# Performance work log

Hardware: AMD Instinct MI355X
Metric: run time of the kernel (lower is better)

Reference implementation:

```python
import jax, jax.numpy as jnp
import numpy as np

N = 1_000_000
B = 4096
L = 4
CC = 3
K = (L + 1) ** 2  # 25


def setup_inputs() -> dict:
    key = jax.random.key(0)
    ks = jax.random.split(key, 20)
    points = jax.random.normal(ks[0], (N, 3), dtype=jnp.float32)
    color = jax.random.uniform(ks[1], (N, 3), dtype=jnp.float32)
    batch = jnp.sort(jax.random.randint(ks[2], (N,), 0, B, dtype=jnp.int64))

    def lin(k, o, i, s):
        return jax.random.normal(k, (o, i), dtype=jnp.float32) * s

    inp = {
        "points": points,
        "color": color,
        "batch": batch,
        # FeatureNet 1x1 conv weights (kernel size 1 -> plain linear)
        "w1": lin(ks[3], 32, 6, 0.4), "b1": jnp.zeros((32,), jnp.float32),
        "w2": lin(ks[4], 128, 32, 0.18), "b2": jnp.zeros((128,), jnp.float32),
        "w3": lin(ks[5], 256, 128, 0.09), "b3": jnp.zeros((256,), jnp.float32),
        # FC head
        "fw1": lin(ks[6], 128, 256, 0.06), "fb1": jnp.zeros((128,), jnp.float32),
        "fw2": lin(ks[7], 64, 128, 0.09), "fb2": jnp.zeros((64,), jnp.float32),
        "fw3": lin(ks[8], K * CC, 64, 0.12), "fb3": jnp.zeros((K * CC,), jnp.float32),
        "coef_mean": jnp.zeros((K, CC), jnp.float32),
        "coef_std": jnp.ones((K, CC), jnp.float32),
    }
    return inp


def reference(points, color, batch, w1, b1, w2, b2, w3, b3,
              fw1, fb1, fw2, fb2, fw3, fb3, coef_mean, coef_std):
    # per-point shared MLP (1x1 convs == linear over channel dim)
    x = jnp.concatenate([points, color], axis=-1)          # [N, 6]
    x = jax.nn.relu(x @ w1.T + b1)                          # [N, 32]
    x = jax.nn.relu(x @ w2.T + b2)                          # [N, 128]
    x = x @ w3.T + b3                                       # [N, 256]
    # scatter_reduce(amax) onto a zeros-initialized target (include_self=True)
    # => per-segment max clamped below at 0; empty segments stay 0.
    seg = jax.ops.segment_max(x, batch, num_segments=B, indices_are_sorted=True)
    x_max = jnp.maximum(seg, 0.0)                           # [B, 256]
    # FC head
    h = jax.nn.relu(x_max @ fw1.T + fb1)                    # [B, 128]
    h = jax.nn.relu(h @ fw2.T + fb2)                        # [B, 64]
    h = h @ fw3.T + fb3                                     # [B, 75]
    out = h.reshape(-1, K, CC) * coef_std + coef_mean       # [B, 25, 3]
    return out
```

## Files before the change

### kernel.cpp

```cpp
#include <hip/hip_runtime.h>
#include <hip/hip_bf16.h>

typedef __attribute__((ext_vector_type(8))) short short8;
typedef __attribute__((ext_vector_type(16))) float f32x16;

union U8 { short8 s; unsigned int u[4]; };

static __device__ __forceinline__ unsigned short f2bf(float f) {
  unsigned int u = __float_as_uint(f);
  u += 0x7fffu + ((u >> 16) & 1u);
  return (unsigned short)(u >> 16);
}
static __device__ __forceinline__ unsigned int cvtpk(float lo, float hi) {
  unsigned int r;
  asm("v_cvt_pk_bf16_f32 %0, %1, %2" : "=v"(r) : "v"(lo), "v"(hi));
  return r;
}
static __device__ __forceinline__ f32x16 MFMA(short8 a, short8 b, f32x16 c) {
  return __builtin_amdgcn_mfma_f32_32x32x16_bf16(a, b, c, 0, 0, 0);
}

__global__ void prep_weights(const float* __restrict__ w1, const float* __restrict__ w2,
                             const float* __restrict__ w3,
                             unsigned short* __restrict__ w1p, unsigned short* __restrict__ w2b,
                             unsigned short* __restrict__ w3b) {
  int i = blockIdx.x * 256 + threadIdx.x;
  if (i < 512) { int c = i >> 4, k = i & 15; w1p[i] = (k < 6) ? f2bf(w1[c * 6 + k]) : (unsigned short)0; }
  if (i < 4096) w2b[i] = f2bf(w2[i]);
  if (i < 32768) w3b[i] = f2bf(w3[i]);
}

__global__ __launch_bounds__(256, 2) void mlp_segmax_mfma(
    const float* __restrict__ points, const float* __restrict__ color,
    const int* __restrict__ batch,
    const unsigned short* __restrict__ w1p, const unsigned short* __restrict__ w2b,
    const unsigned short* __restrict__ w3b,
    const float* __restrict__ b1, const float* __restrict__ b2, const float* __restrict__ b3,
    float* __restrict__ xmax, int N)
{
  __shared__ __align__(16) char smem[73728];
  const int tid  = threadIdx.x;
  const int wv   = tid >> 6;
  const int lane = tid & 63;
  const int g    = lane >> 5;
  const int l31  = lane & 31;
  char* h2base = smem + wv * 16384;
  char* h1base = smem + 65536 + wv * 2048;

  float b1v[16];
#pragma unroll
  for (int r = 0; r < 16; ++r) b1v[r] = b1[(r & 3) + 8 * (r >> 2) + 4 * g];
  unsigned int b2pk[32];
#pragma unroll
  for (int t2 = 0; t2 < 4; ++t2)
#pragma unroll
    for (int q = 0; q < 4; ++q)
#pragma unroll
      for (int h = 0; h < 2; ++h) {
        int ch = 32 * t2 + 8 * q + 4 * g + 2 * h;
        b2pk[t2 * 8 + q * 2 + h] = (unsigned)f2bf(b2[ch]) | ((unsigned)f2bf(b2[ch + 1]) << 16);
      }
  float b3v[8];
#pragma unroll
  for (int t = 0; t < 8; ++t) b3v[t] = b3[32 * t + l31];

  const int wid = blockIdx.x * 4 + wv;
  const long long pstart = (long long)wid * 512;
  int cur = -1;
  float rmax[8];
#pragma unroll
  for (int t = 0; t < 8; ++t) rmax[t] = -INFINITY;

  auto flush = [&]() {
#pragma unroll
    for (int t = 0; t < 8; ++t) {
      float v = fmaxf(rmax[t], __shfl_xor(rmax[t], 32));
      if (lane < 32)
        atomicMax((int*)xmax + cur * 256 + 32 * t + lane, __float_as_int(v));
    }
  };

  for (int it = 0; it < 8; ++it) {
    const long long p0 = pstart + (long long)it * 64;
    if (p0 >= N) break;

    unsigned long long a1p = (unsigned long long)w1p; asm volatile("" : "+s"(a1p));
    unsigned long long a2p = (unsigned long long)w2b; asm volatile("" : "+s"(a2p));
    unsigned long long a3p = (unsigned long long)w3b; asm volatile("" : "+s"(a3p));
    const unsigned short* w1l = (const unsigned short*)a1p;
    const unsigned short* w2l = (const unsigned short*)a2p;
    const unsigned short* w3l = (const unsigned short*)a3p;

#pragma unroll
    for (int s2 = 0; s2 < 2; ++s2) {
      const int p = (int)p0 + 32 * s2 + l31;
      float px = points[p * 3 + 0], py = points[p * 3 + 1], pz = points[p * 3 + 2];
      float cr = color[p * 3 + 0],  cg = color[p * 3 + 1],  cbv = color[p * 3 + 2];
      unsigned int zm = (g == 0) ? 0xffffffffu : 0u;
      U8 bin;
      bin.u[0] = cvtpk(px, py) & zm;
      bin.u[1] = cvtpk(pz, cr) & zm;
      bin.u[2] = cvtpk(cg, cbv) & zm;
      bin.u[3] = 0;
      short8 a1 = *reinterpret_cast<const short8*>(w1l + l31 * 16 + 8 * g);
      f32x16 c1;
#pragma unroll
      for (int r = 0; r < 16; ++r) c1[r] = b1v[r];
      f32x16 d1 = MFMA(a1, bin.s, c1);
#pragma unroll
      for (int q = 0; q < 4; ++q) {
        float f0 = fmaxf(d1[q * 4 + 0], 0.f), f1 = fmaxf(d1[q * 4 + 1], 0.f);
        float f2 = fmaxf(d1[q * 4 + 2], 0.f), f3 = fmaxf(d1[q * 4 + 3], 0.f);
        uint2 w; w.x = cvtpk(f0, f1); w.y = cvtpk(f2, f3);
        *reinterpret_cast<uint2*>(h1base + l31 * 64 + ((q ^ (l31 & 3)) << 4) + 8 * g) = w;
      }
      short8 h1f0 = *reinterpret_cast<const short8*>(h1base + l31 * 64 + (((0 + g) ^ (l31 & 3)) << 4));
      short8 h1f1 = *reinterpret_cast<const short8*>(h1base + l31 * 64 + (((2 + g) ^ (l31 & 3)) << 4));
      const int row = 32 * s2 + l31;
#pragma unroll
      for (int t2 = 0; t2 < 4; ++t2) {
        f32x16 c2;
#pragma unroll
        for (int q = 0; q < 4; ++q) {
          unsigned int pka = b2pk[t2 * 8 + q * 2 + 0], pkb = b2pk[t2 * 8 + q * 2 + 1];
          c2[q * 4 + 0] = __uint_as_float(pka << 16);
          c2[q * 4 + 1] = __uint_as_float(pka & 0xffff0000u);
          c2[q * 4 + 2] = __uint_as_float(pkb << 16);
          c2[q * 4 + 3] = __uint_as_float(pkb & 0xffff0000u);
        }
        short8 a20 = *reinterpret_cast<const short8*>(w2l + (l31 + 32 * t2) * 32 + 8 * g);
        short8 a21 = *reinterpret_cast<const short8*>(w2l + (l31 + 32 * t2) * 32 + 16 + 8 * g);
        f32x16 d2 = MFMA(a20, h1f0, c2);
        d2 = MFMA(a21, h1f1, d2);
#pragma unroll
        for (int q = 0; q < 4; ++q) {
          float f0 = fmaxf(d2[q * 4 + 0], 0.f), f1 = fmaxf(d2[q * 4 + 1], 0.f);
          float f2 = fmaxf(d2[q * 4 + 2], 0.f), f3 = fmaxf(d2[q * 4 + 3], 0.f);
          uint2 w; w.x = cvtpk(f0, f1); w.y = cvtpk(f2, f3);
          int slot = q + 4 * t2;
          *reinterpret_cast<uint2*>(h2base + row * 256 + ((slot ^ (row & 15)) << 4) + 8 * g) = w;
        }
      }
    }

    short8 a3[2][8];
#pragma unroll
    for (int s2 = 0; s2 < 2; ++s2) {
      const int row = 32 * s2 + l31;
#pragma unroll
      for (int k0 = 0; k0 < 8; ++k0)
        a3[s2][k0] = *reinterpret_cast<const short8*>(
            h2base + row * 256 + (((2 * k0 + g) ^ (row & 15)) << 4));
    }

    const int segA = __builtin_amdgcn_readfirstlane(batch[p0]);
    const int segD = __builtin_amdgcn_readfirstlane(batch[p0 + 63]);
    const bool caseU = (segA == segD);
    unsigned int bitsA0 = 0, bitsD0 = 0, bitsA1 = 0, bitsD1 = 0;
    if (caseU) {
      if (segA != cur) {
        if (cur >= 0) flush();
        cur = segA;
#pragma unroll
        for (int t = 0; t < 8; ++t) rmax[t] = -INFINITY;
      }
    } else {
      if (cur >= 0 && cur != segA) flush();
      if (cur != segA) {
#pragma unroll
        for (int t = 0; t < 8; ++t) rmax[t] = -INFINITY;
        cur = segA;
      }
#pragma unroll
      for (int s2 = 0; s2 < 2; ++s2) {
        unsigned int bA = 0, bD = 0;
#pragma unroll
        for (int r = 0; r < 16; ++r) {
          int pr = (int)p0 + 32 * s2 + (r & 3) + 8 * (r >> 2) + 4 * g;
          int bs = batch[pr];
          bA |= (bs == segA) ? (1u << r) : 0u;
          bD |= (bs == segD) ? (1u << r) : 0u;
        }
        if (s2 == 0) { bitsA0 = bA; bitsD0 = bD; } else { bitsA1 = bA; bitsD1 = bD; }
      }
    }

    float m_a[8], m_d[8];
#pragma unroll
    for (int t = 0; t < 8; ++t) {
      f32x16 acc0, acc1;
#pragma unroll
      for (int r = 0; r < 16; ++r) { acc0[r] = b3v[t]; acc1[r] = b3v[t]; }
#pragma unroll
      for (int hh = 0; hh < 2; ++hh) {
        short8 bf[4];
#pragma unroll
        for (int k = 0; k < 4; ++k)
          bf[k] = *reinterpret_cast<const short8*>(
              w3l + (l31 + 32 * t) * 128 + (4 * hh + k) * 16 + 8 * g);
#pragma unroll
        for (int k = 0; k < 4; ++k) {
          acc0 = MFMA(a3[0][4 * hh + k], bf[k], acc0);
          acc1 = MFMA(a3[1][4 * hh + k], bf[k], acc1);
        }
      }
      if (caseU) {
        float m = acc0[0];
#pragma unroll
        for (int r = 1; r < 16; ++r) m = fmaxf(m, acc0[r]);
#pragma unroll
        for (int r = 0; r < 16; ++r) m = fmaxf(m, acc1[r]);
        rmax[t] = fmaxf(rmax[t], m);
      } else {
        float ma = -INFINITY, md = -INFINITY;
#pragma unroll
        for (int r = 0; r < 16; ++r) {
          float v0 = acc0[r], v1 = acc1[r];
          ma = fmaxf(ma, ((bitsA0 >> r) & 1) ? v0 : -INFINITY);
          md = fmaxf(md, ((bitsD0 >> r) & 1) ? v0 : -INFINITY);
          ma = fmaxf(ma, ((bitsA1 >> r) & 1) ? v1 : -INFINITY);
          md = fmaxf(md, ((bitsD1 >> r) & 1) ? v1 : -INFINITY);
        }
        unsigned int rest0 = (~(bitsA0 | bitsD0)) & 0xffffu;
        if (rest0) {
#pragma unroll
          for (int r = 0; r < 16; ++r) if ((rest0 >> r) & 1) {
            int pr = (int)p0 + (r & 3) + 8 * (r >> 2) + 4 * g;
            atomicMax((int*)xmax + batch[pr] * 256 + 32 * t + l31, __float_as_int(acc0[r]));
          }
        }
        unsigned int rest1 = (~(bitsA1 | bitsD1)) & 0xffffu;
        if (rest1) {
#pragma unroll
          for (int r = 0; r < 16; ++r) if ((rest1 >> r) & 1) {
            int pr = (int)p0 + 32 + (r & 3) + 8 * (r >> 2) + 4 * g;
            atomicMax((int*)xmax + batch[pr] * 256 + 32 * t + l31, __float_as_int(acc1[r]));
          }
        }
        m_a[t] = ma; m_d[t] = md;
      }
    }
    if (!caseU) {
#pragma unroll
      for (int t = 0; t < 8; ++t) rmax[t] = fmaxf(rmax[t], m_a[t]);
      flush();
      cur = segD;
#pragma unroll
      for (int t = 0; t < 8; ++t) rmax[t] = m_d[t];
    }
  }
  if (cur >= 0) flush();
}

__global__ __launch_bounds__(256) void head_kernel(
    const float* __restrict__ xmax,
    const float* __restrict__ fw1, const float* __restrict__ fb1,
    const float* __restrict__ fw2, const float* __restrict__ fb2,
    const float* __restrict__ fw3, const float* __restrict__ fb3,
    const float* __restrict__ cmean, const float* __restrict__ cstd,
    float* __restrict__ out, int B)
{
  __shared__ __align__(16) float xm[16][260];
  __shared__ __align__(16) float h1b[16][132];
  __shared__ __align__(16) float h2b[16][68];

  const int t = threadIdx.x;
  const int bbase = blockIdx.x * 16;

  for (int i = t; i < 16 * 256; i += 256) {
    const int bi = i >> 8, k = i & 255;
    const int bb = min(bbase + bi, B - 1);
    xm[bi][k] = xmax[(long long)bb * 256 + k];
  }
  __syncthreads();

  {
    const int bi = t >> 4, oi = t & 15;
    float acc[8];
#pragma unroll
    for (int u = 0; u < 8; ++u) acc[u] = fb1[oi * 8 + u];
    for (int k = 0; k < 256; k += 4) {
      const float4 xv = *reinterpret_cast<const float4*>(&xm[bi][k]);
#pragma unroll
      for (int u = 0; u < 8; ++u) {
        const float4 wv = *reinterpret_cast<const float4*>(fw1 + (oi * 8 + u) * 256 + k);
        acc[u] = fmaf(xv.x, wv.x, acc[u]);
        acc[u] = fmaf(xv.y, wv.y, acc[u]);
        acc[u] = fmaf(xv.z, wv.z, acc[u]);
        acc[u] = fmaf(xv.w, wv.w, acc[u]);
      }
    }
#pragma unroll
    for (int u = 0; u < 8; ++u) h1b[bi][oi * 8 + u] = fmaxf(acc[u], 0.0f);
  }
  __syncthreads();

  {
    const int bi = t >> 4, oi = t & 15;
    float acc[4];
#pragma unroll
    for (int u = 0; u < 4; ++u) acc[u] = fb2[oi * 4 + u];
    for (int k = 0; k < 128; k += 4) {
      const float4 xv = *reinterpret_cast<const float4*>(&h1b[bi][k]);
#pragma unroll
      for (int u = 0; u < 4; ++u) {
        const float4 wv = *reinterpret_cast<const float4*>(fw2 + (oi * 4 + u) * 128 + k);
        acc[u] = fmaf(xv.x, wv.x, acc[u]);
        acc[u] = fmaf(xv.y, wv.y, acc[u]);
        acc[u] = fmaf(xv.z, wv.z, acc[u]);
        acc[u] = fmaf(xv.w, wv.w, acc[u]);
      }
    }
#pragma unroll
    for (int u = 0; u < 4; ++u) h2b[bi][oi * 4 + u] = fmaxf(acc[u], 0.0f);
  }
  __syncthreads();

  for (int i = t; i < 16 * 75; i += 256) {
    const int bi = i / 75, o = i - bi * 75;
    float a = fb3[o];
    for (int k = 0; k < 64; k += 4) {
      const float4 xv = *reinterpret_cast<const float4*>(&h2b[bi][k]);
      const float4 wv = *reinterpret_cast<const float4*>(fw3 + o * 64 + k);
      a = fmaf(xv.x, wv.x, a);
      a = fmaf(xv.y, wv.y, a);
      a = fmaf(xv.z, wv.z, a);
      a = fmaf(xv.w, wv.w, a);
    }
    const int b = bbase + bi;
    if (b < B) out[(long long)b * 75 + o] = fmaf(a, cstd[o], cmean[o]);
  }
}

extern "C" void kernel_launch(void* const* d_in, const int* in_sizes, int n_in,
                              void* d_out, int out_size, void* d_ws, size_t ws_size,
                              hipStream_t stream) {
  const float* points = (const float*)d_in[0];
  const float* color  = (const float*)d_in[1];
  const int*   batch  = (const int*)d_in[2];
  const float* w1  = (const float*)d_in[3];
  const float* b1  = (const float*)d_in[4];
  const float* w2  = (const float*)d_in[5];
  const float* b2  = (const float*)d_in[6];
  const float* w3  = (const float*)d_in[7];
  const float* b3  = (const float*)d_in[8];
  const float* fw1 = (const float*)d_in[9];
  const float* fb1 = (const float*)d_in[10];
  const float* fw2 = (const float*)d_in[11];
  const float* fb2 = (const float*)d_in[12];
  const float* fw3 = (const float*)d_in[13];
  const float* fb3 = (const float*)d_in[14];
  const float* cmean = (const float*)d_in[15];
  const float* cstd  = (const float*)d_in[16];
  float* out = (float*)d_out;

  const int N = in_sizes[2];
  const int B = out_size / 75;

  float* xmax = (float*)d_ws;
  unsigned short* w1p = (unsigned short*)((char*)d_ws + 4194304);
  unsigned short* w2b = (unsigned short*)((char*)d_ws + 4195328);
  unsigned short* w3b = (unsigned short*)((char*)d_ws + 4203520);

  hipMemsetAsync(xmax, 0, (size_t)B * 256 * sizeof(float), stream);
  prep_weights<<<128, 256, 0, stream>>>(w1, w2, w3, w1p, w2b, w3b);

  const int nWaves = 2048;
  mlp_segmax_mfma<<<nWaves / 4, 256, 0, stream>>>(points, color, batch,
                                                  w1p, w2b, w3b, b1, b2, b3, xmax, N);

  head_kernel<<<(B + 15) / 16, 256, 0, stream>>>(xmax, fw1, fb1, fw2, fb2, fw3, fb3,
                                                 cmean, cstd, out, B);
}
```

Measured before the change: 473.0 us.

## Shrink per-wave tile to 32 points, raise occupancy, prefetch next inputs

Each wave now processes 32 points per iteration instead of 64, which halves the layer-2 LDS buffer and the layer-3 accumulators. Launch bounds go from 2 to 4 blocks per CU, and the grid now scales with N instead of being fixed. Next-iteration point, color and batch loads are prefetched into registers. Segment membership now comes from ballots and shuffles instead of repeated global batch reads, and atomics are skipped for non-positive values. The cost is more per-point overhead and more atomics per segment boundary, and the tighter register budget at 4 blocks per CU risks spills.

```diff
diff --git a/kernel.cpp b/kernel.cpp
--- a/kernel.cpp
+++ b/kernel.cpp
@@ -30,7 +30,7 @@
   if (i < 32768) w3b[i] = f2bf(w3[i]);
 }
 
-__global__ __launch_bounds__(256, 2) void mlp_segmax_mfma(
+__global__ __launch_bounds__(256, 4) void mlp_segmax_mfma(
     const float* __restrict__ points, const float* __restrict__ color,
     const int* __restrict__ batch,
     const unsigned short* __restrict__ w1p, const unsigned short* __restrict__ w2b,
@@ -38,18 +38,21 @@
     const float* __restrict__ b1, const float* __restrict__ b2, const float* __restrict__ b3,
     float* __restrict__ xmax, int N)
 {
-  __shared__ __align__(16) char smem[73728];
+  __shared__ __align__(16) char smem[40960];
   const int tid  = threadIdx.x;
   const int wv   = tid >> 6;
   const int lane = tid & 63;
   const int g    = lane >> 5;
   const int l31  = lane & 31;
-  char* h2base = smem + wv * 16384;
-  char* h1base = smem + 65536 + wv * 2048;
-
-  float b1v[16];
-#pragma unroll
-  for (int r = 0; r < 16; ++r) b1v[r] = b1[(r & 3) + 8 * (r >> 2) + 4 * g];
+  char* h2base = smem + wv * 8192;
+  char* h1base = smem + 32768 + wv * 2048;
+
+  unsigned int b1pk[8];
+#pragma unroll
+  for (int rr = 0; rr < 8; ++rr) {
+    int r = 2 * rr, ch = (r & 3) + 8 * (r >> 2) + 4 * g;
+    b1pk[rr] = (unsigned)f2bf(b1[ch]) | ((unsigned)f2bf(b1[ch + 1]) << 16);
+  }
   unsigned int b2pk[32];
 #pragma unroll
   for (int t2 = 0; t2 < 4; ++t2)
@@ -64,133 +67,129 @@
 #pragma unroll
   for (int t = 0; t < 8; ++t) b3v[t] = b3[32 * t + l31];
 
+  const short8 a1 = *reinterpret_cast<const short8*>(w1p + l31 * 16 + 8 * g);
+
   const int wid = blockIdx.x * 4 + wv;
-  const long long pstart = (long long)wid * 512;
   int cur = -1;
   float rmax[8];
 #pragma unroll
   for (int t = 0; t < 8; ++t) rmax[t] = -INFINITY;
 
   auto flush = [&]() {
+    if (cur < 0) return;
 #pragma unroll
     for (int t = 0; t < 8; ++t) {
       float v = fmaxf(rmax[t], __shfl_xor(rmax[t], 32));
-      if (lane < 32)
+      if (lane < 32 && v > 0.0f)
         atomicMax((int*)xmax + cur * 256 + 32 * t + lane, __float_as_int(v));
     }
   };
 
+  const long long wbase = (long long)wid * 256;
+  float n0 = 0, n1 = 0, n2 = 0, n3 = 0, n4 = 0, n5 = 0;
+  int nseg = -2 - lane;
+  if (wbase < (long long)N) {
+    const int p = (int)wbase + l31;
+    n0 = points[p * 3 + 0]; n1 = points[p * 3 + 1]; n2 = points[p * 3 + 2];
+    n3 = color[p * 3 + 0];  n4 = color[p * 3 + 1];  n5 = color[p * 3 + 2];
+    nseg = batch[p];
+  }
+
   for (int it = 0; it < 8; ++it) {
-    const long long p0 = pstart + (long long)it * 64;
-    if (p0 >= N) break;
-
-    unsigned long long a1p = (unsigned long long)w1p; asm volatile("" : "+s"(a1p));
+    const long long base = wbase + (long long)it * 32;
+    if (base >= (long long)N) break;
+
+    const float c0 = n0, c1 = n1, c2 = n2, c3 = n3, c4 = n4, c5 = n5;
+    const int segv = nseg;
+
+    if (base + 32 < (long long)N && it < 7) {
+      const int p = (int)base + 32 + l31;
+      n0 = points[p * 3 + 0]; n1 = points[p * 3 + 1]; n2 = points[p * 3 + 2];
+      n3 = color[p * 3 + 0];  n4 = color[p * 3 + 1];  n5 = color[p * 3 + 2];
+      nseg = batch[p];
+    }
+
     unsigned long long a2p = (unsigned long long)w2b; asm volatile("" : "+s"(a2p));
     unsigned long long a3p = (unsigned long long)w3b; asm volatile("" : "+s"(a3p));
-    const unsigned short* w1l = (const unsigned short*)a1p;
     const unsigned short* w2l = (const unsigned short*)a2p;
     const unsigned short* w3l = (const unsigned short*)a3p;
 
-#pragma unroll
-    for (int s2 = 0; s2 < 2; ++s2) {
-      const int p = (int)p0 + 32 * s2 + l31;
-      float px = points[p * 3 + 0], py = points[p * 3 + 1], pz = points[p * 3 + 2];
-      float cr = color[p * 3 + 0],  cg = color[p * 3 + 1],  cbv = color[p * 3 + 2];
-      unsigned int zm = (g == 0) ? 0xffffffffu : 0u;
-      U8 bin;
-      bin.u[0] = cvtpk(px, py) & zm;
-      bin.u[1] = cvtpk(pz, cr) & zm;
-      bin.u[2] = cvtpk(cg, cbv) & zm;
-      bin.u[3] = 0;
-      short8 a1 = *reinterpret_cast<const short8*>(w1l + l31 * 16 + 8 * g);
-      f32x16 c1;
-#pragma unroll
-      for (int r = 0; r < 16; ++r) c1[r] = b1v[r];
-      f32x16 d1 = MFMA(a1, bin.s, c1);
+    const unsigned int zm = (g == 0) ? 0xffffffffu : 0u;
+    U8 bin;
+    bin.u[0] = cvtpk(c0, c1) & zm;
+    bin.u[1] = cvtpk(c2, c3) & zm;
+    bin.u[2] = cvtpk(c4, c5) & zm;
+    bin.u[3] = 0;
+    f32x16 ci;
+#pragma unroll
+    for (int rr = 0; rr < 8; ++rr) {
+      ci[2 * rr + 0] = __uint_as_float(b1pk[rr] << 16);
+      ci[2 * rr + 1] = __uint_as_float(b1pk[rr] & 0xffff0000u);
+    }
+    f32x16 d1 = MFMA(a1, bin.s, ci);
+#pragma unroll
+    for (int q = 0; q < 4; ++q) {
+      float f0 = fmaxf(d1[q * 4 + 0], 0.f), f1 = fmaxf(d1[q * 4 + 1], 0.f);
+      float f2 = fmaxf(d1[q * 4 + 2], 0.f), f3 = fmaxf(d1[q * 4 + 3], 0.f);
+      uint2 w; w.x = cvtpk(f0, f1); w.y = cvtpk(f2, f3);
+      *reinterpret_cast<uint2*>(h1base + l31 * 64 + ((q ^ (l31 & 3)) << 4) + 8 * g) = w;
+    }
+    const short8 h1f0 = *reinterpret_cast<const short8*>(h1base + l31 * 64 + (((0 + g) ^ (l31 & 3)) << 4));
+    const short8 h1f1 = *reinterpret_cast<const short8*>(h1base + l31 * 64 + (((2 + g) ^ (l31 & 3)) << 4));
+
+#pragma unroll
+    for (int t2 = 0; t2 < 4; ++t2) {
+      f32x16 cc;
 #pragma unroll
       for (int q = 0; q < 4; ++q) {
-        float f0 = fmaxf(d1[q * 4 + 0], 0.f), f1 = fmaxf(d1[q * 4 + 1], 0.f);
-        float f2 = fmaxf(d1[q * 4 + 2], 0.f), f3 = fmaxf(d1[q * 4 + 3], 0.f);
+        unsigned int pka = b2pk[t2 * 8 + q * 2 + 0], pkb = b2pk[t2 * 8 + q * 2 + 1];
+        cc[q * 4 + 0] = __uint_as_float(pka << 16);
+        cc[q * 4 + 1] = __uint_as_float(pka & 0xffff0000u);
+        cc[q * 4 + 2] = __uint_as_float(pkb << 16);
+        cc[q * 4 + 3] = __uint_as_float(pkb & 0xffff0000u);
+      }
+      short8 a20 = *reinterpret_cast<const short8*>(w2l + (l31 + 32 * t2) * 32 + 8 * g);
+      short8 a21 = *reinterpret_cast<const short8*>(w2l + (l31 + 32 * t2) * 32 + 16 + 8 * g);
+      f32x16 d2 = MFMA(a20, h1f0, cc);
+      d2 = MFMA(a21, h1f1, d2);
+#pragma unroll
+      for (int q = 0; q < 4; ++q) {
+        float f0 = fmaxf(d2[q * 4 + 0], 0.f), f1 = fmaxf(d2[q * 4 + 1], 0.f);
+        float f2 = fmaxf(d2[q * 4 + 2], 0.f), f3 = fmaxf(d2[q * 4 + 3], 0.f);
         uint2 w; w.x = cvtpk(f0, f1); w.y = cvtpk(f2, f3);
-        *reinterpret_cast<uint2*>(h1base + l31 * 64 + ((q ^ (l31 & 3)) << 4) + 8 * g) = w;
-      }
-      short8 h1f0 = *reinterpret_cast<const short8*>(h1base + l31 * 64 + (((0 + g) ^ (l31 & 3)) << 4));
-      short8 h1f1 = *reinterpret_cast<const short8*>(h1base + l31 * 64 + (((2 + g) ^ (l31 & 3)) << 4));
-      const int row = 32 * s2 + l31;
-#pragma unroll
-      for (int t2 = 0; t2 < 4; ++t2) {
-        f32x16 c2;
-#pragma unroll
-        for (int q = 0; q < 4; ++q) {
-          unsigned int pka = b2pk[t2 * 8 + q * 2 + 0], pkb = b2pk[t2 * 8 + q * 2 + 1];
-          c2[q * 4 + 0] = __uint_as_float(pka << 16);
-          c2[q * 4 + 1] = __uint_as_float(pka & 0xffff0000u);
-          c2[q * 4 + 2] = __uint_as_float(pkb << 16);
-          c2[q * 4 + 3] = __uint_as_float(pkb & 0xffff0000u);
-        }
-        short8 a20 = *reinterpret_cast<const short8*>(w2l + (l31 + 32 * t2) * 32 + 8 * g);
-        short8 a21 = *reinterpret_cast<const short8*>(w2l + (l31 + 32 * t2) * 32 + 16 + 8 * g);
-        f32x16 d2 = MFMA(a20, h1f0, c2);
-        d2 = MFMA(a21, h1f1, d2);
-#pragma unroll
-        for (int q = 0; q < 4; ++q) {
-          float f0 = fmaxf(d2[q * 4 + 0], 0.f), f1 = fmaxf(d2[q * 4 + 1], 0.f);
-          float f2 = fmaxf(d2[q * 4 + 2], 0.f), f3 = fmaxf(d2[q * 4 + 3], 0.f);
-          uint2 w; w.x = cvtpk(f0, f1); w.y = cvtpk(f2, f3);
-          int slot = q + 4 * t2;
-          *reinterpret_cast<uint2*>(h2base + row * 256 + ((slot ^ (row & 15)) << 4) + 8 * g) = w;
-        }
-      }
-    }
-
-    short8 a3[2][8];
-#pragma unroll
-    for (int s2 = 0; s2 < 2; ++s2) {
-      const int row = 32 * s2 + l31;
-#pragma unroll
-      for (int k0 = 0; k0 < 8; ++k0)
-        a3[s2][k0] = *reinterpret_cast<const short8*>(
-            h2base + row * 256 + (((2 * k0 + g) ^ (row & 15)) << 4));
-    }
-
-    const int segA = __builtin_amdgcn_readfirstlane(batch[p0]);
-    const int segD = __builtin_amdgcn_readfirstlane(batch[p0 + 63]);
+        int slot = q + 4 * t2;
+        *reinterpret_cast<uint2*>(h2base + l31 * 256 + ((slot ^ (l31 & 15)) << 4) + 8 * g) = w;
+      }
+    }
+
+    short8 a3[8];
+#pragma unroll
+    for (int k0 = 0; k0 < 8; ++k0)
+      a3[k0] = *reinterpret_cast<const short8*>(
+          h2base + l31 * 256 + (((2 * k0 + g) ^ (l31 & 15)) << 4));
+
+    const int segA = __builtin_amdgcn_readfirstlane(segv);
+    const int segD = __shfl(segv, 31);
     const bool caseU = (segA == segD);
-    unsigned int bitsA0 = 0, bitsD0 = 0, bitsA1 = 0, bitsD1 = 0;
-    if (caseU) {
-      if (segA != cur) {
-        if (cur >= 0) flush();
-        cur = segA;
-#pragma unroll
-        for (int t = 0; t < 8; ++t) rmax[t] = -INFINITY;
-      }
-    } else {
-      if (cur >= 0 && cur != segA) flush();
-      if (cur != segA) {
-#pragma unroll
-        for (int t = 0; t < 8; ++t) rmax[t] = -INFINITY;
-        cur = segA;
-      }
-#pragma unroll
-      for (int s2 = 0; s2 < 2; ++s2) {
-        unsigned int bA = 0, bD = 0;
-#pragma unroll
-        for (int r = 0; r < 16; ++r) {
-          int pr = (int)p0 + 32 * s2 + (r & 3) + 8 * (r >> 2) + 4 * g;
-          int bs = batch[pr];
-          bA |= (bs == segA) ? (1u << r) : 0u;
-          bD |= (bs == segD) ? (1u << r) : 0u;
-        }
-        if (s2 == 0) { bitsA0 = bA; bitsD0 = bD; } else { bitsA1 = bA; bitsD1 = bD; }
-      }
-    }
-
-    float m_a[8], m_d[8];
+    if (segA != cur) {
+      flush();
+#pragma unroll
+      for (int t = 0; t < 8; ++t) rmax[t] = -INFINITY;
+      cur = segA;
+    }
+    unsigned int bA = 0, bD = 0;
+    bool restAny = false;
+    if (!caseU) {
+      bA = (unsigned int)__ballot(segv == segA);
+      bD = (unsigned int)__ballot(segv == segD);
+      restAny = ((bA | bD) != 0xffffffffu);
+    }
+
 #pragma unroll
     for (int t = 0; t < 8; ++t) {
-      f32x16 acc0, acc1;
-#pragma unroll
-      for (int r = 0; r < 16; ++r) { acc0[r] = b3v[t]; acc1[r] = b3v[t]; }
+      f32x16 acc;
+#pragma unroll
+      for (int r = 0; r < 16; ++r) acc[r] = b3v[t];
 #pragma unroll
       for (int hh = 0; hh < 2; ++hh) {
         short8 bf[4];
@@ -199,57 +198,46 @@
           bf[k] = *reinterpret_cast<const short8*>(
               w3l + (l31 + 32 * t) * 128 + (4 * hh + k) * 16 + 8 * g);
 #pragma unroll
-        for (int k = 0; k < 4; ++k) {
-          acc0 = MFMA(a3[0][4 * hh + k], bf[k], acc0);
-          acc1 = MFMA(a3[1][4 * hh + k], bf[k], acc1);
-        }
+        for (int k = 0; k < 4; ++k) acc = MFMA(a3[4 * hh + k], bf[k], acc);
       }
       if (caseU) {
-        float m = acc0[0];
-#pragma unroll
-        for (int r = 1; r < 16; ++r) m = fmaxf(m, acc0[r]);
-#pragma unroll
-        for (int r = 0; r < 16; ++r) m = fmaxf(m, acc1[r]);
+        float m = acc[0];
+#pragma unroll
+        for (int r = 1; r < 16; ++r) m = fmaxf(m, acc[r]);
         rmax[t] = fmaxf(rmax[t], m);
       } else {
         float ma = -INFINITY, md = -INFINITY;
 #pragma unroll
         for (int r = 0; r < 16; ++r) {
-          float v0 = acc0[r], v1 = acc1[r];
-          ma = fmaxf(ma, ((bitsA0 >> r) & 1) ? v0 : -INFINITY);
-          md = fmaxf(md, ((bitsD0 >> r) & 1) ? v0 : -INFINITY);
-          ma = fmaxf(ma, ((bitsA1 >> r) & 1) ? v1 : -INFINITY);
-          md = fmaxf(md, ((bitsD1 >> r) & 1) ? v1 : -INFINITY);
+          const int idx = (r & 3) + 8 * (r >> 2) + 4 * g;
+          const unsigned int bit = 1u << idx;
+          const float v = acc[r];
+          ma = fmaxf(ma, (bA & bit) ? v : -INFINITY);
+          md = fmaxf(md, (bD & bit) ? v : -INFINITY);
         }
-        unsigned int rest0 = (~(bitsA0 | bitsD0)) & 0xffffu;
-        if (rest0) {
-#pragma unroll
-          for (int r = 0; r < 16; ++r) if ((rest0 >> r) & 1) {
-            int pr = (int)p0 + (r & 3) + 8 * (r >> 2) + 4 * g;
-            atomicMax((int*)xmax + batch[pr] * 256 + 32 * t + l31, __float_as_int(acc0[r]));
+        if (restAny) {
+#pragma unroll
+          for (int r = 0; r < 16; ++r) {
+            const int idx = (r & 3) + 8 * (r >> 2) + 4 * g;
+            const unsigned int bit = 1u << idx;
+            if (!((bA | bD) & bit)) {
+              const int sid = __shfl(segv, idx);
+              const float v = acc[r];
+              if (sid >= 0 && v > 0.0f)
+                atomicMax((int*)xmax + sid * 256 + 32 * t + l31, __float_as_int(v));
+            }
           }
         }
-        unsigned int rest1 = (~(bitsA1 | bitsD1)) & 0xffffu;
-        if (rest1) {
-#pragma unroll
-          for (int r = 0; r < 16; ++r) if ((rest1 >> r) & 1) {
-            int pr = (int)p0 + 32 + (r & 3) + 8 * (r >> 2) + 4 * g;
-            atomicMax((int*)xmax + batch[pr] * 256 + 32 * t + l31, __float_as_int(acc1[r]));
-          }
-        }
-        m_a[t] = ma; m_d[t] = md;
-      }
-    }
-    if (!caseU) {
-#pragma unroll
-      for (int t = 0; t < 8; ++t) rmax[t] = fmaxf(rmax[t], m_a[t]);
-      flush();
-      cur = segD;
-#pragma unroll
-      for (int t = 0; t < 8; ++t) rmax[t] = m_d[t];
-    }
-  }
-  if (cur >= 0) flush();
+        float va = fmaxf(rmax[t], ma);
+        va = fmaxf(va, __shfl_xor(va, 32));
+        if (lane < 32 && va > 0.0f)
+          atomicMax((int*)xmax + segA * 256 + 32 * t + l31, __float_as_int(va));
+        rmax[t] = md;
+      }
+    }
+    if (!caseU) cur = segD;
+  }
+  flush();
 }
 
 __global__ __launch_bounds__(256) void head_kernel(
@@ -365,9 +353,10 @@
   hipMemsetAsync(xmax, 0, (size_t)B * 256 * sizeof(float), stream);
   prep_weights<<<128, 256, 0, stream>>>(w1, w2, w3, w1p, w2b, w3b);
 
-  const int nWaves = 2048;
-  mlp_segmax_mfma<<<nWaves / 4, 256, 0, stream>>>(points, color, batch,
-                                                  w1p, w2b, w3b, b1, b2, b3, xmax, N);
+  const int nWaves  = (N + 255) / 256;
+  const int nBlocks = (nWaves + 3) / 4;
+  mlp_segmax_mfma<<<nBlocks, 256, 0, stream>>>(points, color, batch,
+                                               w1p, w2b, w3b, b1, b2, b3, xmax, N);
 
   head_kernel<<<(B + 15) / 16, 256, 0, stream>>>(xmax, fw1, fb1, fw2, fb2, fw3, fb3,
                                                  cmean, cstd, out, B);
```

New measurement: 812.0 us. +71.7%, slower.
